# Performance work log

Hardware: AMD Instinct MI355X
Metric: run time of the kernel (lower is better)

The kernel has to match this reference:

```python
import jax, jax.numpy as jnp
import numpy as np

V, E, H = 32000, 512, 1024
B, T = 32, 64

def setup_inputs() -> dict:
    key = jax.random.key(0)
    ks = jax.random.split(key, 8)
    return {
        "x": jax.random.randint(ks[0], (B, T), 0, V, dtype=jnp.int32),
        "state_h": jax.random.normal(ks[1], (B, H), dtype=jnp.float32),
        "state_c": jax.random.normal(ks[2], (B, H), dtype=jnp.float32),
        "emb_table": jax.random.normal(ks[3], (V, E), dtype=jnp.float32) * 0.02,
        "W": jax.random.normal(ks[4], (E, 4 * H), dtype=jnp.float32) * (1.0 / np.sqrt(E)),
        "U": jax.random.normal(ks[5], (H, 4 * H), dtype=jnp.float32) * (1.0 / np.sqrt(H)),
        "b": jnp.zeros((4 * H,), dtype=jnp.float32),
        "dense_W": jax.random.normal(ks[6], (H, V), dtype=jnp.float32) * (1.0 / np.sqrt(H)),
        "dense_b": jnp.zeros((V,), dtype=jnp.float32),
    }

def _lstm(emb, h0, c0, W, U, b):
    # Precompute input projections for all timesteps: [B,T,4H]
    xW = jnp.einsum('bte,eg->btg', emb, W) + b
    def step(carry, xw_t):
        h, c = carry
        z = xw_t + h @ U  # [B,4H]
        i, f, g, o = jnp.split(z, 4, axis=-1)  # Keras gate order i,f,c,o
        i = jax.nn.sigmoid(i)
        f = jax.nn.sigmoid(f)
        g = jnp.tanh(g)
        o = jax.nn.sigmoid(o)
        c = f * c + i * g
        h = o * jnp.tanh(c)
        return (h, c), h
    (h, c), hs = jax.lax.scan(step, (h0, c0), xW.transpose(1, 0, 2))
    return hs.transpose(1, 0, 2), h, c  # [B,T,H], [B,H], [B,H]

def reference(x, state_h, state_c, emb_table, W, U, b, dense_W, dense_b):
    emb = emb_table[x]  # [B,T,E]
    seq, h, c = _lstm(emb, state_h, state_c, W, U, b)
    logits = jnp.einsum('bth,hv->btv', seq, dense_W) + dense_b  # [B,T,V]
    return logits, h, c
```

## Files before the change

kernel.cpp:

```cpp
#include <hip/hip_runtime.h>

typedef unsigned short u16;
typedef __bf16 bf16x8 __attribute__((ext_vector_type(8)));
typedef float f32x4 __attribute__((ext_vector_type(4)));

#define T_STEPS 64
#define BATCH 32
#define HDIM 1024
#define EDIM 512
#define VDIM 32000
#define GDIM 4096

__device__ __forceinline__ u16 f2b(float v) {
  unsigned x = __float_as_uint(v);
  return (u16)((x + 0x7fffu + ((x >> 16) & 1u)) >> 16);
}

__device__ __forceinline__ void gload16(const void* g, void* l) {
  __builtin_amdgcn_global_load_lds(
      (const __attribute__((address_space(1))) void*)g,
      (__attribute__((address_space(3))) void*)l, 16, 0, 0);
}

__device__ __forceinline__ f32x4 mfma16(bf16x8 a, bf16x8 b, f32x4 c) {
  return __builtin_amdgcn_mfma_f32_16x16x32_bf16(a, b, c, 0, 0, 0);
}


__global__ __launch_bounds__(256) void gather_emb_k(
    const int* __restrict__ x, const float* __restrict__ emb,
    u16* __restrict__ A) {
  int bt = blockIdx.x;
  int tok = x[bt];
  const float* src = emb + (size_t)tok * EDIM;
  u16* dst = A + (size_t)bt * EDIM;
  for (int i = threadIdx.x; i < EDIM; i += 256) dst[i] = f2b(src[i]);
}

__global__ __launch_bounds__(256) void transpose_cvt_k(
    const float* __restrict__ in, u16* __restrict__ out, int K, int N) {
  __shared__ u16 tile[64][72];
  int n0 = blockIdx.x * 64, k0 = blockIdx.y * 64;
  int tid = threadIdx.x;
  int cr = tid >> 6;
  int cc = tid & 63;
#pragma unroll
  for (int rr = 0; rr < 16; ++rr) {
    int r = rr * 4 + cr;
    tile[cc][r] = f2b(in[(size_t)(k0 + r) * N + n0 + cc]);
  }
  __syncthreads();
#pragma unroll
  for (int rr = 0; rr < 16; ++rr) {
    int r = rr * 4 + cr;
    out[(size_t)(n0 + r) * K + k0 + cc] = tile[r][cc];
  }
}

__global__ __launch_bounds__(256) void transpose_cvt_permU_k(
    const float* __restrict__ in, u16* __restrict__ out) {
  const int K = HDIM, N = GDIM;
  __shared__ u16 tile[64][72];
  int n0 = blockIdx.x * 64, k0 = blockIdx.y * 64;
  int tid = threadIdx.x;
  int cr = tid >> 6;
  int cc = tid & 63;
#pragma unroll
  for (int rr = 0; rr < 16; ++rr) {
    int r = rr * 4 + cr;
    tile[cc][r] = f2b(in[(size_t)(k0 + r) * N + n0 + cc]);
  }
  __syncthreads();
#pragma unroll
  for (int rr = 0; rr < 16; ++rr) {
    int r = rr * 4 + cr;
    int n = n0 + r;
    int g = n >> 10, c = n & 1023;
    int pn = ((c >> 2) << 4) + (g << 2) + (c & 3);
    out[(size_t)pn * K + k0 + cc] = tile[r][cc];
  }
}

__global__ __launch_bounds__(256) void init_state_k(
    const float* __restrict__ h0, const float* __restrict__ c0,
    u16* __restrict__ h0b, float* __restrict__ c_ws) {
  int i = blockIdx.x * 256 + threadIdx.x;
  h0b[i] = f2b(h0[i]);
  c_ws[i] = c0[i];
}


__global__ __launch_bounds__(256) void gemm_bf16_k(
    const u16* __restrict__ A,
    const u16* __restrict__ BT,
    const float* __restrict__ bias,
    float* __restrict__ C,
    int M, int N, int K) {
  __shared__ u16 As[128 * 64];
  __shared__ u16 Bs[128 * 64];
  const int tid = threadIdx.x;
  const int w = tid >> 6, lane = tid & 63;
  const int lo16 = lane & 15, hi4 = lane >> 4;
  const int nmb = gridDim.y;
  const int bid = blockIdx.y * gridDim.x + blockIdx.x;
  const int m0 = (bid % nmb) * 128, n0 = (bid / nmb) * 128;
  const int wr = w >> 1, wc = w & 1;
  f32x4 acc[4][4] = {};

  const int srow = lane >> 3;
  const int scol = (lane & 7) * 8;

  for (int k0 = 0; k0 < K; k0 += 64) {
    __syncthreads();
#pragma unroll
    for (int r = 0; r < 4; ++r) {
      int blkrow = (r * 4 + w) * 8 + srow;
      gload16(A + (size_t)(m0 + blkrow) * K + k0 + scol,
              As + (r * 4 + w) * 512);
      gload16(BT + (size_t)(n0 + blkrow) * K + k0 + scol,
              Bs + (r * 4 + w) * 512);
    }
    __syncthreads();

    bf16x8 af[4][2], bfr[4][2];
#pragma unroll
    for (int mi = 0; mi < 4; ++mi)
#pragma unroll
      for (int kk = 0; kk < 2; ++kk)
        af[mi][kk] = *reinterpret_cast<const bf16x8*>(
            As + (wr * 64 + mi * 16 + lo16) * 64 + kk * 32 + hi4 * 8);
#pragma unroll
    for (int nj = 0; nj < 4; ++nj)
#pragma unroll
      for (int kk = 0; kk < 2; ++kk)
        bfr[nj][kk] = *reinterpret_cast<const bf16x8*>(
            Bs + (wc * 64 + nj * 16 + lo16) * 64 + kk * 32 + hi4 * 8);
#pragma unroll
    for (int mi = 0; mi < 4; ++mi)
#pragma unroll
      for (int nj = 0; nj < 4; ++nj)
#pragma unroll
        for (int kk = 0; kk < 2; ++kk)
          acc[mi][nj] = mfma16(af[mi][kk], bfr[nj][kk], acc[mi][nj]);
  }

  const int row0 = m0 + wr * 64, col0 = n0 + wc * 64;
#pragma unroll
  for (int mi = 0; mi < 4; ++mi) {
#pragma unroll
    for (int nj = 0; nj < 4; ++nj) {
      int col = col0 + nj * 16 + lo16;
      float bv = bias ? bias[col] : 0.f;
#pragma unroll
      for (int j = 0; j < 4; ++j) {
        int row = row0 + mi * 16 + hi4 * 4 + j;
        C[(size_t)row * N + col] = acc[mi][nj][j] + bv;
      }
    }
  }
}


__global__ __launch_bounds__(256) void lstm_step2_k(
    const float* __restrict__ xW,
    const u16* __restrict__ h_src,
    int h_stride,
    const u16* __restrict__ UT2,
    float* __restrict__ c_ws,
    u16* __restrict__ seq,
    float* __restrict__ out_hc,
    int t) {
  __shared__ float Zs[4][16][17];
  const int tid = threadIdx.x;
  const int w = tid >> 6, lane = tid & 63;
  const int lo16 = lane & 15, hi4 = lane >> 4;
  const int zt = blockIdx.x >> 1;
  const int bt = blockIdx.x & 1;

  const u16* arow = h_src + (size_t)(bt * 16 + lo16) * h_stride;
  const u16* brow = UT2 + (size_t)(zt * 16 + lo16) * HDIM;

  f32x4 acc = {};
#pragma unroll
  for (int kc = 0; kc < 8; ++kc) {
    int k = w * 256 + kc * 32 + hi4 * 8;
    bf16x8 a = *reinterpret_cast<const bf16x8*>(arow + k);
    bf16x8 b = *reinterpret_cast<const bf16x8*>(brow + k);
    acc = mfma16(a, b, acc);
  }
#pragma unroll
  for (int j = 0; j < 4; ++j) Zs[w][hi4 * 4 + j][lo16] = acc[j];
  __syncthreads();

  if (tid < 64) {
    int bb = tid >> 2, j = tid & 3;
    int b = bt * 16 + bb;
    int hcol = zt * 4 + j;
    float z[4];
#pragma unroll
    for (int g = 0; g < 4; ++g) {
      float s = xW[(size_t)(b * T_STEPS + t) * GDIM + g * HDIM + hcol];
#pragma unroll
      for (int ww = 0; ww < 4; ++ww) s += Zs[ww][bb][g * 4 + j];
      z[g] = s;
    }
    size_t cidx = (size_t)b * HDIM + hcol;
    float c_old = c_ws[cidx];
    float ig = 1.f / (1.f + __expf(-z[0]));
    float fg = 1.f / (1.f + __expf(-z[1]));
    float gg = tanhf(z[2]);
    float og = 1.f / (1.f + __expf(-z[3]));
    float cn = fg * c_old + ig * gg;
    float hn = og * tanhf(cn);
    c_ws[cidx] = cn;
    seq[(size_t)(b * T_STEPS + t) * HDIM + hcol] = f2b(hn);
    if (out_hc) {
      out_hc[cidx] = hn;
      out_hc[BATCH * HDIM + cidx] = cn;
    }
  }
}


extern "C" void kernel_launch(void* const* d_in, const int* in_sizes, int n_in,
                              void* d_out, int out_size, void* d_ws,
                              size_t ws_size, hipStream_t stream) {
  const int* x = (const int*)d_in[0];
  const float* state_h = (const float*)d_in[1];
  const float* state_c = (const float*)d_in[2];
  const float* emb = (const float*)d_in[3];
  const float* W = (const float*)d_in[4];
  const float* U = (const float*)d_in[5];
  const float* bvec = (const float*)d_in[6];
  const float* dW = (const float*)d_in[7];
  const float* db = (const float*)d_in[8];
  float* out = (float*)d_out;
  char* ws = (char*)d_ws;

  size_t off = 0;
  auto alloc = [&](size_t bytes) {
    void* p = ws + off;
    off += (bytes + 255) & ~(size_t)255;
    return p;
  };
  u16* A_emb = (u16*)alloc(2048ull * EDIM * 2);
  u16* WbT   = (u16*)alloc((size_t)GDIM * EDIM * 2);
  u16* UT2   = (u16*)alloc((size_t)GDIM * HDIM * 2);
  u16* DbT   = (u16*)alloc((size_t)VDIM * HDIM * 2);
  float* xW  = (float*)alloc(2048ull * GDIM * 4);
  u16* seq   = (u16*)alloc(2048ull * HDIM * 2);
  u16* h0b   = (u16*)alloc((size_t)BATCH * HDIM * 2);
  float* c_ws = (float*)alloc((size_t)BATCH * HDIM * 4);
  if (off > ws_size) return;

  gather_emb_k<<<2048, 256, 0, stream>>>(x, emb, A_emb);
  transpose_cvt_k<<<dim3(GDIM / 64, EDIM / 64), 256, 0, stream>>>(W, WbT, EDIM, GDIM);
  transpose_cvt_permU_k<<<dim3(GDIM / 64, HDIM / 64), 256, 0, stream>>>(U, UT2);
  transpose_cvt_k<<<dim3(VDIM / 64, HDIM / 64), 256, 0, stream>>>(dW, DbT, HDIM, VDIM);
  init_state_k<<<128, 256, 0, stream>>>(state_h, state_c, h0b, c_ws);

  gemm_bf16_k<<<dim3(GDIM / 128, 2048 / 128), 256, 0, stream>>>(
      A_emb, WbT, bvec, xW, 2048, GDIM, EDIM);

  for (int t = 0; t < T_STEPS; ++t) {
    const u16* h_src = (t == 0) ? h0b : (seq + (size_t)(t - 1) * HDIM);
    int h_stride = (t == 0) ? HDIM : T_STEPS * HDIM;
    float* outhc = (t == T_STEPS - 1) ? (out + 65536000ull) : nullptr;
    lstm_step2_k<<<512, 256, 0, stream>>>(xW, h_src, h_stride, UT2, c_ws, seq,
                                          outhc, t);
  }

  gemm_bf16_k<<<dim3(VDIM / 128, 2048 / 128), 256, 0, stream>>>(
      seq, DbT, db, out, 2048, VDIM, HDIM);
}
```

Before: 736.9 us.

## Add pipelined 256x256 GEMM for logits, vectorize transposes, prefetch xW in LSTM step

Replaces the 128x128 logits GEMM with a new 256x256 tile, 512-thread kernel that double-buffers LDS through direct global-to-LDS loads, uses XOR-swizzled LDS offsets, a grouped block order and s_setprio around the MFMA phases. The weight transpose kernels now write 16-byte vectors instead of 2-byte scalars, with padding changed to keep alignment. The LSTM step kernel loads its xW gate inputs before the recurrent MFMA so the global load latency overlaps the matrix work. The aim is better reuse and latency hiding in the dominant vocabulary GEMM, at the cost of heavy LDS use (128KB per block) and hand-tuned waitcnt ordering.

After: 647.1 us. -12.2%, faster.

```diff
diff --git a/kernel.cpp b/kernel.cpp
--- a/kernel.cpp
+++ b/kernel.cpp
@@ -3,6 +3,7 @@
 typedef unsigned short u16;
 typedef __bf16 bf16x8 __attribute__((ext_vector_type(8)));
 typedef float f32x4 __attribute__((ext_vector_type(4)));
+typedef u16 u16x8 __attribute__((ext_vector_type(8)));
 
 #define T_STEPS 64
 #define BATCH 32
@@ -39,7 +40,7 @@
 
 __global__ __launch_bounds__(256) void transpose_cvt_k(
     const float* __restrict__ in, u16* __restrict__ out, int K, int N) {
-  __shared__ u16 tile[64][72];
+  __shared__ u16 tile[64][80];
   int n0 = blockIdx.x * 64, k0 = blockIdx.y * 64;
   int tid = threadIdx.x;
   int cr = tid >> 6;
@@ -50,17 +51,19 @@
     tile[cc][r] = f2b(in[(size_t)(k0 + r) * N + n0 + cc]);
   }
   __syncthreads();
-#pragma unroll
-  for (int rr = 0; rr < 16; ++rr) {
-    int r = rr * 4 + cr;
-    out[(size_t)(n0 + r) * K + k0 + cc] = tile[r][cc];
+  int wr2 = tid >> 3, c8 = (tid & 7) * 8;
+#pragma unroll
+  for (int rr = 0; rr < 2; ++rr) {
+    int r = rr * 32 + wr2;
+    *reinterpret_cast<u16x8*>(&out[(size_t)(n0 + r) * K + k0 + c8]) =
+        *reinterpret_cast<const u16x8*>(&tile[r][c8]);
   }
 }
 
 __global__ __launch_bounds__(256) void transpose_cvt_permU_k(
     const float* __restrict__ in, u16* __restrict__ out) {
   const int K = HDIM, N = GDIM;
-  __shared__ u16 tile[64][72];
+  __shared__ u16 tile[64][80];
   int n0 = blockIdx.x * 64, k0 = blockIdx.y * 64;
   int tid = threadIdx.x;
   int cr = tid >> 6;
@@ -71,13 +74,15 @@
     tile[cc][r] = f2b(in[(size_t)(k0 + r) * N + n0 + cc]);
   }
   __syncthreads();
-#pragma unroll
-  for (int rr = 0; rr < 16; ++rr) {
-    int r = rr * 4 + cr;
+  int wr2 = tid >> 3, c8 = (tid & 7) * 8;
+#pragma unroll
+  for (int rr = 0; rr < 2; ++rr) {
+    int r = rr * 32 + wr2;
     int n = n0 + r;
     int g = n >> 10, c = n & 1023;
     int pn = ((c >> 2) << 4) + (g << 2) + (c & 3);
-    out[(size_t)pn * K + k0 + cc] = tile[r][cc];
+    *reinterpret_cast<u16x8*>(&out[(size_t)pn * K + k0 + c8]) =
+        *reinterpret_cast<const u16x8*>(&tile[r][c8]);
   }
 }
 
@@ -91,10 +96,8 @@
 
 
 __global__ __launch_bounds__(256) void gemm_bf16_k(
-    const u16* __restrict__ A,
-    const u16* __restrict__ BT,
-    const float* __restrict__ bias,
-    float* __restrict__ C,
+    const u16* __restrict__ A, const u16* __restrict__ BT,
+    const float* __restrict__ bias, float* __restrict__ C,
     int M, int N, int K) {
   __shared__ u16 As[128 * 64];
   __shared__ u16 Bs[128 * 64];
@@ -156,6 +159,151 @@
         int row = row0 + mi * 16 + hi4 * 4 + j;
         C[(size_t)row * N + col] = acc[mi][nj][j] + bv;
       }
+    }
+  }
+}
+
+
+#define STG_A(dst, h, kb)                                              \
+  do {                                                                 \
+    gload16(Abytes + offA[h][0] + (kb), (dst) + (h) * 16384 + w * 1024); \
+    gload16(Abytes + offA[h][1] + (kb),                                \
+            (dst) + (h) * 16384 + 8192 + w * 1024);                    \
+  } while (0)
+#define STG_B(dst, h, kb)                                              \
+  do {                                                                 \
+    gload16(Bbytes + offB[h][0] + (kb),                                \
+            (dst) + 32768 + (h) * 16384 + w * 1024);                   \
+    gload16(Bbytes + offB[h][1] + (kb),                                \
+            (dst) + 32768 + (h) * 16384 + 8192 + w * 1024);            \
+  } while (0)
+#define VMW4 asm volatile("s_waitcnt vmcnt(4)" ::: "memory")
+
+#define PHASE(cur, mih, njh, STG, WAIT)                                   \
+  do {                                                                    \
+    bf16x8 af[4][2], bfr[2][2];                                           \
+    _Pragma("unroll") for (int u = 0; u < 4; ++u) {                       \
+      af[u][0] = *reinterpret_cast<const bf16x8*>((cur) +                 \
+                                                  aoff[(mih)*4 + u][0]);  \
+      af[u][1] = *reinterpret_cast<const bf16x8*>((cur) +                 \
+                                                  aoff[(mih)*4 + u][1]);  \
+    }                                                                     \
+    _Pragma("unroll") for (int v = 0; v < 2; ++v) {                       \
+      bfr[v][0] = *reinterpret_cast<const bf16x8*>((cur) +                \
+                                                   boff[(njh)*2 + v][0]); \
+      bfr[v][1] = *reinterpret_cast<const bf16x8*>((cur) +                \
+                                                   boff[(njh)*2 + v][1]); \
+    }                                                                     \
+    STG;                                                                  \
+    __builtin_amdgcn_s_barrier();                                         \
+    asm volatile("s_waitcnt lgkmcnt(0)" ::: "memory");                    \
+    __builtin_amdgcn_s_setprio(1);                                        \
+    _Pragma("unroll") for (int u = 0; u < 4; ++u)                         \
+        _Pragma("unroll") for (int v = 0; v < 2; ++v) {                   \
+      acc[(mih)*4 + u][(njh)*2 + v] =                                     \
+          mfma16(af[u][0], bfr[v][0], acc[(mih)*4 + u][(njh)*2 + v]);     \
+      acc[(mih)*4 + u][(njh)*2 + v] =                                     \
+          mfma16(af[u][1], bfr[v][1], acc[(mih)*4 + u][(njh)*2 + v]);     \
+    }                                                                     \
+    __builtin_amdgcn_s_setprio(0);                                        \
+    WAIT;                                                                 \
+    __builtin_amdgcn_s_barrier();                                         \
+  } while (0)
+
+__global__ __launch_bounds__(512, 2) void gemm256_k(
+    const u16* __restrict__ A,
+    const u16* __restrict__ BT,
+    const float* __restrict__ bias,
+    float* __restrict__ C,
+    int M, int N, int K) {
+  __shared__ __attribute__((aligned(1024))) char smem[131072];
+  const int tid = threadIdx.x;
+  const int w = tid >> 6, lane = tid & 63;
+  const int lo16 = lane & 15, hi4 = lane >> 4;
+  const int wr = w >> 2, wc = w & 3;
+
+  const int cpx = gridDim.x >> 3;
+  const int bid = blockIdx.x;
+  const int swz = (bid & 7) * cpx + (bid >> 3);
+  const int nmb = M >> 8;
+  const int m0 = (swz % nmb) << 8, n0 = (swz / nmb) << 8;
+
+  const char* Abytes = (const char*)A;
+  const char* Bbytes = (const char*)BT;
+  const int K2 = K * 2;
+
+  int offA[2][2], offB[2][2];
+#pragma unroll
+  for (int h = 0; h < 2; ++h)
+#pragma unroll
+    for (int i = 0; i < 2; ++i) {
+      int o = h * 16384 + (i * 512 + tid) * 16;
+      int s = o >> 10, q = o & 1023;
+      int qp = q ^ (((q >> 9) & 1) << 5);
+      int row = ((s >> 1) << 4) + (qp >> 6);
+      int colb = ((s & 1) << 6) + (qp & 63);
+      offA[h][i] = (m0 + row) * K2 + colb;
+      offB[h][i] = (n0 + row) * K2 + colb;
+    }
+
+  int aoff[8][2], boff[4][2];
+#pragma unroll
+  for (int mi = 0; mi < 8; ++mi)
+#pragma unroll
+    for (int kk = 0; kk < 2; ++kk) {
+      int r = (mi >> 2) * 128 + wr * 64 + (mi & 3) * 16 + lo16;
+      int q = (r & 15) * 64 + hi4 * 16;
+      int qs = q ^ (((q >> 9) & 1) << 5);
+      aoff[mi][kk] = (((r >> 4) << 1) + kk) * 1024 + qs;
+    }
+#pragma unroll
+  for (int nj = 0; nj < 4; ++nj)
+#pragma unroll
+    for (int kk = 0; kk < 2; ++kk) {
+      int r = (nj >> 1) * 128 + wc * 32 + (nj & 1) * 16 + lo16;
+      int q = (r & 15) * 64 + hi4 * 16;
+      int qs = q ^ (((q >> 9) & 1) << 5);
+      boff[nj][kk] = 32768 + (((r >> 4) << 1) + kk) * 1024 + qs;
+    }
+
+  f32x4 acc[8][4] = {};
+  char* const bd = smem;
+  char* const bo = smem + 65536;
+
+  STG_A(bd, 0, 0);
+  STG_B(bd, 0, 0);
+  STG_A(bd, 1, 0);
+  STG_B(bd, 1, 0);
+  STG_A(bo, 0, 128);
+  STG_B(bo, 0, 128);
+  VMW4;
+  __builtin_amdgcn_s_barrier();
+
+  const int NITER = K >> 7;
+  for (int it = 0; it < NITER; ++it) {
+    const int k1 = (it * 128 + 64) * 2;
+    const int k2 = min(it * 128 + 128, K - 64) * 2;
+    const int k3 = min(it * 128 + 192, K - 64) * 2;
+    PHASE(bd, 0, 0, STG_A(bo, 1, k1), ((void)0));
+    PHASE(bd, 0, 1, STG_B(bo, 1, k1), ((void)0));
+    PHASE(bd, 1, 0, STG_A(bd, 0, k2), ((void)0));
+    PHASE(bd, 1, 1, STG_B(bd, 0, k2), VMW4);
+    PHASE(bo, 0, 0, STG_A(bd, 1, k2), ((void)0));
+    PHASE(bo, 0, 1, STG_B(bd, 1, k2), ((void)0));
+    PHASE(bo, 1, 0, STG_A(bo, 0, k3), ((void)0));
+    PHASE(bo, 1, 1, STG_B(bo, 0, k3), VMW4);
+  }
+
+#pragma unroll
+  for (int mi = 0; mi < 8; ++mi) {
+    int row = m0 + (mi >> 2) * 128 + wr * 64 + (mi & 3) * 16 + hi4 * 4;
+#pragma unroll
+    for (int nj = 0; nj < 4; ++nj) {
+      int col = n0 + (nj >> 1) * 128 + wc * 32 + (nj & 1) * 16 + lo16;
+      float bv = bias ? bias[col] : 0.f;
+#pragma unroll
+      for (int j = 0; j < 4; ++j)
+        C[(size_t)(row + j) * N + col] = acc[mi][nj][j] + bv;
     }
   }
 }
@@ -177,6 +325,17 @@
   const int zt = blockIdx.x >> 1;
   const int bt = blockIdx.x & 1;
 
+  const int bb = tid >> 2, jg = tid & 3;
+  float xw0 = 0.f, xw1 = 0.f, xw2 = 0.f, xw3 = 0.f;
+  if (tid < 64) {
+    const float* xrow =
+        xW + (size_t)((bt * 16 + bb) * T_STEPS + t) * GDIM + zt * 4 + jg;
+    xw0 = xrow[0];
+    xw1 = xrow[1024];
+    xw2 = xrow[2048];
+    xw3 = xrow[3072];
+  }
+
   const u16* arow = h_src + (size_t)(bt * 16 + lo16) * h_stride;
   const u16* brow = UT2 + (size_t)(zt * 16 + lo16) * HDIM;
 
@@ -193,17 +352,13 @@
   __syncthreads();
 
   if (tid < 64) {
-    int bb = tid >> 2, j = tid & 3;
     int b = bt * 16 + bb;
-    int hcol = zt * 4 + j;
-    float z[4];
-#pragma unroll
-    for (int g = 0; g < 4; ++g) {
-      float s = xW[(size_t)(b * T_STEPS + t) * GDIM + g * HDIM + hcol];
-#pragma unroll
-      for (int ww = 0; ww < 4; ++ww) s += Zs[ww][bb][g * 4 + j];
-      z[g] = s;
-    }
+    int hcol = zt * 4 + jg;
+    float z[4] = {xw0, xw1, xw2, xw3};
+#pragma unroll
+    for (int g = 0; g < 4; ++g)
+#pragma unroll
+      for (int ww = 0; ww < 4; ++ww) z[g] += Zs[ww][bb][g * 4 + jg];
     size_t cidx = (size_t)b * HDIM + hcol;
     float c_old = c_ws[cidx];
     float ig = 1.f / (1.f + __expf(-z[0]));
@@ -270,6 +425,6 @@
                                           outhc, t);
   }
 
-  gemm_bf16_k<<<dim3(VDIM / 128, 2048 / 128), 256, 0, stream>>>(
+  gemm256_k<<<dim3((2048 / 256) * (VDIM / 256)), 512, 0, stream>>>(
       seq, DbT, db, out, 2048, VDIM, HDIM);
 }
```
